# Optimization experiments

Measured on AMD Instinct MI355X. Metric: run time of the kernel, lower is better.

The kernel has to match this reference:

```python
import jax, jax.numpy as jnp
import numpy as np

B, N, C = 8, 1024, 768
H = 12
D = C // H            # 64
HID = int(C * 4.0)    # 3072
SCALE = D ** -0.5
EPS_LN = 1e-5
EPS_BN = 1e-5


def _layernorm(x, g, b):
    mu = jnp.mean(x, axis=-1, keepdims=True)
    var = jnp.mean(jnp.square(x - mu), axis=-1, keepdims=True)
    return (x - mu) * jax.lax.rsqrt(var + EPS_LN) * g + b


def setup_inputs() -> dict:
    key = jax.random.key(0)
    ks = jax.random.split(key, 12)
    s = lambda fan: 1.0 / np.sqrt(fan)
    inp = {
        "inputs": jax.random.normal(ks[0], (B, N, C), jnp.float32),
        "ln1_g": jnp.ones((C,), jnp.float32),
        "ln1_b": jnp.zeros((C,), jnp.float32),
        # nn.Linear(dim, 3*dim, bias=False)
        "qkv_w": jax.random.uniform(ks[1], (3 * C, C), jnp.float32, -s(C), s(C)),
        # nn.Conv2d(H, H, 1, 1) head-mixing matrix
        "conv_w": jax.random.uniform(ks[2], (H, H), jnp.float32, -s(H), s(H)),
        "conv_b": jax.random.uniform(ks[3], (H,), jnp.float32, -s(H), s(H)),
        # BatchNorm2d(H) in eval mode: affine params + running stats
        "bn_g": jnp.ones((H,), jnp.float32),
        "bn_b": jnp.zeros((H,), jnp.float32),
        "bn_rm": jnp.zeros((H,), jnp.float32),
        "bn_rv": jnp.ones((H,), jnp.float32),
        "proj_w": jax.random.uniform(ks[4], (C, C), jnp.float32, -s(C), s(C)),
        "proj_b": jax.random.uniform(ks[5], (C,), jnp.float32, -s(C), s(C)),
        "ln2_g": jnp.ones((C,), jnp.float32),
        "ln2_b": jnp.zeros((C,), jnp.float32),
        "fc1_w": jax.random.uniform(ks[6], (HID, C), jnp.float32, -s(C), s(C)),
        "fc1_b": jax.random.uniform(ks[7], (HID,), jnp.float32, -s(C), s(C)),
        "fc2_w": jax.random.uniform(ks[8], (C, HID), jnp.float32, -s(HID), s(HID)),
        "fc2_b": jax.random.uniform(ks[9], (C,), jnp.float32, -s(HID), s(HID)),
    }
    return inp


def reference(inputs, ln1_g, ln1_b, qkv_w, conv_w, conv_b, bn_g, bn_b, bn_rm, bn_rv,
              proj_w, proj_b, ln2_g, ln2_b, fc1_w, fc1_b, fc2_w, fc2_b):
    # adjust_ratio = 1.0, dropouts are identity (inference), BN uses running stats (eval)
    x_ln = _layernorm(inputs, ln1_g, ln1_b)
    qkv = (x_ln @ qkv_w.T).reshape(B, N, 3, H, D).transpose(2, 0, 3, 1, 4)
    q, k, v = qkv[0], qkv[1], qkv[2]
    attn = jax.nn.softmax(jnp.einsum('bhnd,bhmd->bhnm', q, k) * SCALE, axis=-1)
    # 1x1 conv across heads then BatchNorm2d (eval) * reatten_scale(=1.0)
    attn = jnp.einsum('oh,bhnm->bonm', conv_w, attn) + conv_b[None, :, None, None]
    bn_scale = bn_g * jax.lax.rsqrt(bn_rv + EPS_BN)
    attn = (attn - bn_rm[None, :, None, None]) * bn_scale[None, :, None, None] \
        + bn_b[None, :, None, None]
    attn_next = attn
    out = jnp.einsum('bhnm,bhmd->bhnd', attn, v).transpose(0, 2, 1, 3).reshape(B, N, C)
    out = out @ proj_w.T + proj_b
    x = inputs + out
    h = _layernorm(x, ln2_g, ln2_b)
    h = jax.nn.gelu(h @ fc1_w.T + fc1_b, approximate=False)
    x = x + (h @ fc2_w.T + fc2_b)
    return (x, attn_next)
```

## Files before the change

kernel.cpp:

```cpp
#include <hip/hip_runtime.h>
#include <cmath>

#define B_   8
#define N_   1024
#define C_   768
#define H_   12
#define D_   64
#define HID_ 3072
#define M_   8192

using frag  = __attribute__((ext_vector_type(8))) short;
using f32x4 = __attribute__((ext_vector_type(4))) float;
using s4v   = __attribute__((ext_vector_type(4))) short;

__device__ __forceinline__ short f2bf(float x) {
    union { float f; unsigned u; } v; v.f = x;
    unsigned r = (v.u + 0x7FFFu + ((v.u >> 16) & 1u)) >> 16;
    return (short)r;
}
__device__ __forceinline__ float gelu_exact(float x) {
    return 0.5f * x * (1.0f + erff(x * 0.70710678118654752f));
}
__device__ __forceinline__ void gload16(const void* g, void* l) {
    __builtin_amdgcn_global_load_lds(
        (const __attribute__((address_space(1))) void*)g,
        (__attribute__((address_space(3))) void*)l, 16, 0, 0);
}

__device__ __forceinline__ int2 swz_xy() {
    const int gx = gridDim.x;
    const int nwg = gx * gridDim.y;
    const int orig = blockIdx.y * gx + blockIdx.x;
    const int q = nwg >> 3, r = nwg & 7;
    const int xcd = orig & 7;
    const int base = (xcd < r) ? xcd * (q + 1) : r * (q + 1) + (xcd - r) * q;
    const int wgid = base + (orig >> 3);
    int2 v; v.x = wgid % gx; v.y = wgid / gx;
    return v;
}

#define NW0 (3 * C_ * C_)
#define NW1 (C_ * C_)
#define NW2 (HID_ * C_)
#define NW3 (C_ * HID_)
__global__ __launch_bounds__(256)
void cvt_weights(const float* __restrict__ s0, const float* __restrict__ s1,
                 const float* __restrict__ s2, const float* __restrict__ s3,
                 short* __restrict__ dst)
{
    long i = ((long)blockIdx.x * 256 + threadIdx.x) * 4;
    const float* s; long off;
    if      (i < NW0)             { s = s0; off = i; }
    else if (i < NW0 + NW1)       { s = s1; off = i - NW0; }
    else if (i < NW0 + NW1 + NW2) { s = s2; off = i - NW0 - NW1; }
    else                          { s = s3; off = i - NW0 - NW1 - NW2; }
    float4 u = *(const float4*)(s + off);
    s4v o; o[0] = f2bf(u.x); o[1] = f2bf(u.y); o[2] = f2bf(u.z); o[3] = f2bf(u.w);
    *(s4v*)(dst + i) = o;
}

__global__ __launch_bounds__(256)
void ln_bf16(const float* __restrict__ x, const float* __restrict__ g,
             const float* __restrict__ b, short* __restrict__ y)
{
    __shared__ float red[256];
    const long row = blockIdx.x;
    const float* xr = x + row * C_;
    short* yr = y + row * C_;
    const int t = threadIdx.x;
    float v0 = xr[t], v1 = xr[t + 256], v2 = xr[t + 512];
    red[t] = v0 + v1 + v2;
    __syncthreads();
    for (int o = 128; o > 0; o >>= 1) { if (t < o) red[t] += red[t + o]; __syncthreads(); }
    const float mu = red[0] * (1.0f / 768.0f);
    __syncthreads();
    const float d0 = v0 - mu, d1 = v1 - mu, d2 = v2 - mu;
    red[t] = d0 * d0 + d1 * d1 + d2 * d2;
    __syncthreads();
    for (int o = 128; o > 0; o >>= 1) { if (t < o) red[t] += red[t + o]; __syncthreads(); }
    const float rstd = rsqrtf(red[0] * (1.0f / 768.0f) + 1e-5f);
    yr[t]       = f2bf(d0 * rstd * g[t]       + b[t]);
    yr[t + 256] = f2bf(d1 * rstd * g[t + 256] + b[t + 256]);
    yr[t + 512] = f2bf(d2 * rstd * g[t + 512] + b[t + 512]);
}

template<int BM, int BN, int WGM, int WGN, bool AF32, bool OUTF32,
         bool ACT_GELU, bool STATS, bool CW, bool NTC, int GMODE>
__global__ __launch_bounds__(256)
void gemm_mfma(const void* __restrict__ Ap, int lda, long sAb, long sAh,
               const short* __restrict__ Bp, int ldb, long sBb, long sBh,
               const float* __restrict__ bias,
               const float* __restrict__ res, int ldres,
               void* __restrict__ Cp, int ldc, long sCb, long sCh,
               float2* __restrict__ st,
               int K, float alpha)
{
    constexpr int FM = BM / (WGM * 16), FN = BN / (WGN * 16);
    __shared__ short As[BM * 64];
    __shared__ short Bs[BN * 64];
    const int tid = threadIdx.x;
    const int wid = tid >> 6, lane = tid & 63;
    int bx, by, z;
    if constexpr (GMODE == 1) {
        const int nwg = gridDim.x;
        const int qc = nwg >> 3;
        const int wg = (blockIdx.x & 7) * qc + (blockIdx.x >> 3);
        bx = 0; by = wg & 7; z = wg >> 3;
    } else {
        int2 v = swz_xy(); bx = v.x; by = v.y; z = blockIdx.z;
    }
    const int zb = z / H_, zh = z - zb * H_;
    const long m0 = (long)by * BM;
    const int  n0 = bx * BN;
    const short* Bb = Bp + zb * sBb + zh * sBh + (long)n0 * ldb;
    const short* Abh = nullptr; const float* Afh = nullptr;
    if constexpr (AF32) Afh = (const float*)Ap + zb * sAb + zh * sAh + m0 * lda;
    else                Abh = (const short*)Ap + zb * sAb + zh * sAh + m0 * lda;
    f32x4 acc[FM][FN] = {};
    const int wr = wid / WGN, wc = wid - wr * WGN;
    const int srow = lane >> 3;
    const int schunk = (lane & 7) ^ srow;

    for (int k0 = 0; k0 < K; k0 += 64) {
        if constexpr (!AF32) {
            for (int g = wid; g < BM / 8; g += 4)
                gload16(Abh + (long)(g * 8 + srow) * lda + k0 + schunk * 8, &As[g * 512]);
        } else {
            const int r = tid >> 1, h2 = tid & 1;
            const float* sp = Afh + (long)r * lda + k0 + h2 * 32;
            #pragma unroll
            for (int j = 0; j < 4; ++j) {
                float4 u0 = *(const float4*)(sp + j * 8);
                float4 u1 = *(const float4*)(sp + j * 8 + 4);
                frag w;
                w[0] = f2bf(u0.x); w[1] = f2bf(u0.y); w[2] = f2bf(u0.z); w[3] = f2bf(u0.w);
                w[4] = f2bf(u1.x); w[5] = f2bf(u1.y); w[6] = f2bf(u1.z); w[7] = f2bf(u1.w);
                *(frag*)&As[r * 64 + ((h2 * 4 + j) ^ (r & 7)) * 8] = w;
            }
        }
        for (int g = wid; g < BN / 8; g += 4)
            gload16(Bb + (long)(g * 8 + srow) * ldb + k0 + schunk * 8, &Bs[g * 512]);
        __syncthreads();
        #pragma unroll
        for (int kk = 0; kk < 2; ++kk) {
            frag a[FM], b[FN];
            #pragma unroll
            for (int fm = 0; fm < FM; ++fm) {
                const int r = wr * FM * 16 + fm * 16 + (lane & 15);
                const int ph = (kk * 4 + (lane >> 4)) ^ (r & 7);
                a[fm] = *(const frag*)&As[r * 64 + ph * 8];
            }
            #pragma unroll
            for (int fn = 0; fn < FN; ++fn) {
                const int r = wc * FN * 16 + fn * 16 + (lane & 15);
                const int ph = (kk * 4 + (lane >> 4)) ^ (r & 7);
                b[fn] = *(const frag*)&Bs[r * 64 + ph * 8];
            }
            #pragma unroll
            for (int fm = 0; fm < FM; ++fm)
                #pragma unroll
                for (int fn = 0; fn < FN; ++fn)
                    acc[fm][fn] = __builtin_amdgcn_mfma_f32_16x16x32_bf16(a[fm], b[fn], acc[fm][fn], 0, 0, 0);
        }
        __syncthreads();
    }

    if constexpr (CW) {
        float* Cf = (float*)Cp; short* Cs = (short*)Cp;
        const long cbase = zb * sCb + zh * sCh;
        #pragma unroll
        for (int fm = 0; fm < FM; ++fm) {
            #pragma unroll
            for (int fn = 0; fn < FN; ++fn) {
                const long rg = m0 + wr * FM * 16 + fm * 16 + ((lane >> 4) * 4);
                const int  cg = n0 + wc * FN * 16 + fn * 16 + (lane & 15);
                const float bv = bias ? bias[cg] : 0.0f;
                #pragma unroll
                for (int q = 0; q < 4; ++q) {
                    const long row = rg + q;
                    float v = acc[fm][fn][q] * alpha + bv;
                    if (res) v += res[row * (long)ldres + cg];
                    if constexpr (ACT_GELU) v = gelu_exact(v);
                    if constexpr (OUTF32) {
                        if constexpr (NTC) __builtin_nontemporal_store(v, &Cf[cbase + row * ldc + cg]);
                        else               Cf[cbase + row * ldc + cg] = v;
                    } else {
                        Cs[cbase + row * ldc + cg] = f2bf(v);
                    }
                }
            }
        }
    }

    if constexpr (STATS) {
        float* sred = (float*)As;
        float tmax[FM][4];
        #pragma unroll
        for (int fm = 0; fm < FM; ++fm)
            #pragma unroll
            for (int q = 0; q < 4; ++q) {
                float v = acc[fm][0][q];
                #pragma unroll
                for (int fn = 1; fn < FN; ++fn) v = fmaxf(v, acc[fm][fn][q]);
                v *= alpha;
                v = fmaxf(v, __shfl_xor(v, 1));
                v = fmaxf(v, __shfl_xor(v, 2));
                v = fmaxf(v, __shfl_xor(v, 4));
                v = fmaxf(v, __shfl_xor(v, 8));
                const int r = wr * FM * 16 + fm * 16 + (lane >> 4) * 4 + q;
                if ((lane & 15) == 0) sred[wc * BM + r] = v;
            }
        __syncthreads();
        #pragma unroll
        for (int fm = 0; fm < FM; ++fm)
            #pragma unroll
            for (int q = 0; q < 4; ++q) {
                const int r = wr * FM * 16 + fm * 16 + (lane >> 4) * 4 + q;
                tmax[fm][q] = fmaxf(sred[r], sred[BM + r]);
            }
        __syncthreads();
        #pragma unroll
        for (int fm = 0; fm < FM; ++fm)
            #pragma unroll
            for (int q = 0; q < 4; ++q) {
                float e = 0.0f;
                #pragma unroll
                for (int fn = 0; fn < FN; ++fn)
                    e += __expf(acc[fm][fn][q] * alpha - tmax[fm][q]);
                e += __shfl_xor(e, 1);
                e += __shfl_xor(e, 2);
                e += __shfl_xor(e, 4);
                e += __shfl_xor(e, 8);
                const int r = wr * FM * 16 + fm * 16 + (lane >> 4) * 4 + q;
                if ((lane & 15) == 0) sred[wc * BM + r] = e;
            }
        __syncthreads();
        if (wc == 0) {
            #pragma unroll
            for (int fm = 0; fm < FM; ++fm)
                #pragma unroll
                for (int q = 0; q < 4; ++q) {
                    const int r = wr * FM * 16 + fm * 16 + (lane >> 4) * 4 + q;
                    if ((lane & 15) == 0) {
                        float2 o; o.x = tmax[fm][q]; o.y = sred[r] + sred[BM + r];
                        st[((long)z * N_ + m0 + r) * 8 + bx] = o;
                    }
                }
        }
    }
}

__global__ __launch_bounds__(256)
void qksm(const short* __restrict__ qkvb, const float2* __restrict__ st,
          float* __restrict__ attn,
          const float* __restrict__ cw, const float* __restrict__ cb,
          const float* __restrict__ bg, const float* __restrict__ bb,
          const float* __restrict__ brm, const float* __restrict__ brv)
{
    __shared__ short qs[H_ * 16 * 64];
    __shared__ short ks[2][64 * 64];
    __shared__ float smx[H_][16], sinv[H_][16];
    __shared__ float coef[H_][H_], baseA[H_], scA[H_];
    const int tid = threadIdx.x, wid = tid >> 6, lane = tid & 63;

    const int wg = (blockIdx.x & 7) * 1024 + (blockIdx.x >> 3);
    const int b = wg >> 10, nblk = (wg >> 4) & 63, mblk = wg & 15;
    const int n0 = nblk * 16, m0 = mblk * 64;

    if (tid < H_) {
        const float s = bg[tid] * rsqrtf(brv[tid] + 1e-5f);
        scA[tid] = s;
        baseA[tid] = (cb[tid] - brm[tid]) * s + bb[tid];
    }
    __syncthreads();
    if (tid < H_ * H_) coef[tid / H_][tid % H_] = cw[tid] * scA[tid / H_];
    if (tid < 192) {
        const int h = tid >> 4, r = tid & 15;
        const float2* sp = st + ((long)(b * H_ + h) * N_ + n0 + r) * 8;
        float2 sv[8];
        #pragma unroll
        for (int i = 0; i < 8; ++i) sv[i] = sp[i];
        float gm = sv[0].x;
        #pragma unroll
        for (int i = 1; i < 8; ++i) gm = fmaxf(gm, sv[i].x);
        float gs = 0.0f;
        #pragma unroll
        for (int i = 0; i < 8; ++i) gs += sv[i].y * __expf(sv[i].x - gm);
        smx[h][r] = gm;
        sinv[h][r] = 1.0f / gs;
    }
    __syncthreads();

    const int srow = lane >> 3, schunk = (lane & 7) ^ srow;
    const short* qbase = qkvb + (long)(b * N_ + n0) * (3 * C_);
    for (int g = wid; g < 24; g += 4) {
        const int fr = g * 8 + srow;
        gload16(qbase + (long)(fr & 15) * (3 * C_) + (fr >> 4) * 64 + schunk * 8,
                &qs[g * 512]);
    }
    const short* kbase = qkvb + C_ + (long)(b * N_ + m0) * (3 * C_);
    for (int g = wid; g < 8; g += 4) {
        const int fr = g * 8 + srow;
        gload16(kbase + (long)fr * (3 * C_) + schunk * 8, &ks[0][g * 512]);
    }

    float macc[H_][4] = {};
    const int rowb = (lane >> 4) * 4;
    const int colw = wid * 16 + (lane & 15);

    for (int h = 0; h < H_; ++h) {
        asm volatile("s_waitcnt vmcnt(0)" ::: "memory");
        __builtin_amdgcn_sched_barrier(0);
        __builtin_amdgcn_s_barrier();
        if (h < H_ - 1) {
            for (int g = wid; g < 8; g += 4) {
                const int fr = g * 8 + srow;
                gload16(kbase + (long)fr * (3 * C_) + (h + 1) * 64 + schunk * 8,
                        &ks[(h + 1) & 1][g * 512]);
            }
        }
        f32x4 acc = {};
        const int afr = h * 16 + (lane & 15);
        const int bfr = colw;
        #pragma unroll
        for (int kk = 0; kk < 2; ++kk) {
            const frag a  = *(const frag*)&qs[afr * 64 + (((kk * 4 + (lane >> 4)) ^ (afr & 7))) * 8];
            const frag bv = *(const frag*)&ks[h & 1][bfr * 64 + (((kk * 4 + (lane >> 4)) ^ (bfr & 7))) * 8];
            acc = __builtin_amdgcn_mfma_f32_16x16x32_bf16(a, bv, acc, 0, 0, 0);
        }
        #pragma unroll
        for (int q = 0; q < 4; ++q) {
            const float e = __expf(acc[q] * 0.125f - smx[h][rowb + q]) * sinv[h][rowb + q];
            #pragma unroll
            for (int o = 0; o < H_; ++o) macc[o][q] += coef[o][h] * e;
        }
    }

    #pragma unroll
    for (int o = 0; o < H_; ++o) {
        float* ap = attn + ((long)(b * H_ + o) << 20) + ((long)(n0 + rowb) << 10) + m0 + colw;
        #pragma unroll
        for (int q = 0; q < 4; ++q)
            __builtin_nontemporal_store(macc[o][q] + baseA[o], ap + ((long)q << 10));
    }
}

__global__ __launch_bounds__(256)
void vtrans(const short* __restrict__ qkv, short* __restrict__ vT)
{
    __shared__ short tile[64][72];
    const int bh = blockIdx.x;
    const int n0 = blockIdx.y * 64;
    const int b = bh / H_, h = bh - b * H_;
    const short* src = qkv + (long)b * N_ * (3 * C_) + 2 * C_ + h * D_;
    const int t = threadIdx.x;
    {
        const int r = t >> 2, c = (t & 3) * 16;
        const short* sp = src + (long)(n0 + r) * (3 * C_) + c;
        #pragma unroll
        for (int j = 0; j < 16; j++) tile[r][c + j] = sp[j];
    }
    __syncthreads();
    {
        const int d = t >> 2, c = (t & 3) * 16;
        short* dp = vT + (long)bh * (D_ * N_) + (long)d * N_ + n0 + c;
        #pragma unroll
        for (int j = 0; j < 16; j++) dp[j] = tile[c + j][d];
    }
}

extern "C" void kernel_launch(void* const* d_in, const int* in_sizes, int n_in,
                              void* d_out, int out_size, void* d_ws, size_t ws_size,
                              hipStream_t stream)
{
    const float* inp    = (const float*)d_in[0];
    const float* ln1_g  = (const float*)d_in[1];
    const float* ln1_b  = (const float*)d_in[2];
    const float* qkv_w  = (const float*)d_in[3];
    const float* conv_w = (const float*)d_in[4];
    const float* conv_b = (const float*)d_in[5];
    const float* bn_g   = (const float*)d_in[6];
    const float* bn_b   = (const float*)d_in[7];
    const float* bn_rm  = (const float*)d_in[8];
    const float* bn_rv  = (const float*)d_in[9];
    const float* proj_w = (const float*)d_in[10];
    const float* proj_b = (const float*)d_in[11];
    const float* ln2_g  = (const float*)d_in[12];
    const float* ln2_b  = (const float*)d_in[13];
    const float* fc1_w  = (const float*)d_in[14];
    const float* fc1_b  = (const float*)d_in[15];
    const float* fc2_w  = (const float*)d_in[16];
    const float* fc2_b  = (const float*)d_in[17];

    float* outx = (float*)d_out;
    float* attn = outx + (long)M_ * C_;

    char* w = (char*)d_ws;
    short* wqkv  = (short*)w;  w += (long)NW0 * 2;
    short* wproj = (short*)w;  w += (long)NW1 * 2;
    short* wfc1  = (short*)w;  w += (long)NW2 * 2;
    short* wfc2  = (short*)w;  w += (long)NW3 * 2;
    short* xln   = (short*)w;  w += (long)M_ * C_ * 2;
    short* qkvb  = (short*)w;
    short* hbuf  = qkvb;       w += (long)M_ * HID_ * 2;
    short* vT    = (short*)w;  w += (long)B_ * H_ * D_ * N_ * 2;
    short* Obf   = (short*)w;  w += (long)M_ * C_ * 2;
    float* xres  = (float*)w;  w += (long)M_ * C_ * 4;
    float2* st   = (float2*)w; w += (long)B_ * H_ * N_ * 8 * 8;

    cvt_weights<<<(NW0 + NW1 + NW2 + NW3) / 1024, 256, 0, stream>>>(
        qkv_w, proj_w, fc1_w, fc2_w, wqkv);

    ln_bf16<<<M_, 256, 0, stream>>>(inp, ln1_g, ln1_b, xln);

    gemm_mfma<128, 128, 2, 2, false, false, false, false, true, false, 0>
        <<<dim3(18, 64, 1), 256, 0, stream>>>(
        xln, C_, 0, 0, wqkv, C_, 0, 0, nullptr, nullptr, 0,
        qkvb, 3 * C_, 0, 0, nullptr, C_, 1.0f);

    vtrans<<<dim3(B_ * H_, 16), 256, 0, stream>>>(qkvb, vT);

    gemm_mfma<128, 128, 2, 2, false, false, false, true, false, false, 0>
        <<<dim3(8, 8, 96), 256, 0, stream>>>(
        qkvb,      3 * C_, (long)N_ * 3 * C_, D_,
        qkvb + C_, 3 * C_, (long)N_ * 3 * C_, D_,
        nullptr, nullptr, 0,
        nullptr, N_, 0, 0, st, D_, 0.125f);

    qksm<<<8192, 256, 0, stream>>>(qkvb, st, attn,
                                   conv_w, conv_b, bn_g, bn_b, bn_rm, bn_rv);

    gemm_mfma<128, 64, 4, 1, true, false, false, false, true, false, 1>
        <<<dim3(768, 1, 1), 256, 0, stream>>>(
        attn, N_, (long)H_ * N_ * N_, (long)N_ * N_,
        vT, N_, (long)H_ * D_ * N_, (long)D_ * N_,
        nullptr, nullptr, 0,
        Obf, C_, (long)N_ * C_, D_, nullptr, N_, 1.0f);

    gemm_mfma<128, 64, 4, 1, false, true, false, false, true, false, 0>
        <<<dim3(12, 64, 1), 256, 0, stream>>>(
        Obf, C_, 0, 0, wproj, C_, 0, 0, proj_b, inp, C_,
        xres, C_, 0, 0, nullptr, C_, 1.0f);

    ln_bf16<<<M_, 256, 0, stream>>>(xres, ln2_g, ln2_b, xln);

    gemm_mfma<128, 128, 2, 2, false, false, true, false, true, false, 0>
        <<<dim3(24, 64, 1), 256, 0, stream>>>(
        xln, C_, 0, 0, wfc1, C_, 0, 0, fc1_b, nullptr, 0,
        hbuf, HID_, 0, 0, nullptr, C_, 1.0f);

    gemm_mfma<128, 64, 4, 1, false, true, false, false, true, true, 0>
        <<<dim3(12, 64, 1), 256, 0, stream>>>(
        hbuf, HID_, 0, 0, wfc2, HID_, 0, 0, fc2_b, xres, C_,
        outx, C_, 0, 0, nullptr, HID_, 1.0f);
}
```

Measured before the change: 545.0 us.

## Emit bf16 copy of attention in qksm and feed PV GEMM from it

```diff
diff --git a/kernel.cpp b/kernel.cpp
--- a/kernel.cpp
+++ b/kernel.cpp
@@ -84,10 +84,10 @@
     yr[t + 512] = f2bf(d2 * rstd * g[t + 512] + b[t + 512]);
 }
 
-template<int BM, int BN, int WGM, int WGN, bool AF32, bool OUTF32,
+template<int BM, int BN, int WGM, int WGN, bool OUTF32,
          bool ACT_GELU, bool STATS, bool CW, bool NTC, int GMODE>
 __global__ __launch_bounds__(256)
-void gemm_mfma(const void* __restrict__ Ap, int lda, long sAb, long sAh,
+void gemm_mfma(const short* __restrict__ Ap, int lda, long sAb, long sAh,
                const short* __restrict__ Bp, int ldb, long sBb, long sBh,
                const float* __restrict__ bias,
                const float* __restrict__ res, int ldres,
@@ -112,32 +112,16 @@
     const int zb = z / H_, zh = z - zb * H_;
     const long m0 = (long)by * BM;
     const int  n0 = bx * BN;
+    const short* Ab = Ap + zb * sAb + zh * sAh + m0 * lda;
     const short* Bb = Bp + zb * sBb + zh * sBh + (long)n0 * ldb;
-    const short* Abh = nullptr; const float* Afh = nullptr;
-    if constexpr (AF32) Afh = (const float*)Ap + zb * sAb + zh * sAh + m0 * lda;
-    else                Abh = (const short*)Ap + zb * sAb + zh * sAh + m0 * lda;
     f32x4 acc[FM][FN] = {};
     const int wr = wid / WGN, wc = wid - wr * WGN;
     const int srow = lane >> 3;
     const int schunk = (lane & 7) ^ srow;
 
     for (int k0 = 0; k0 < K; k0 += 64) {
-        if constexpr (!AF32) {
-            for (int g = wid; g < BM / 8; g += 4)
-                gload16(Abh + (long)(g * 8 + srow) * lda + k0 + schunk * 8, &As[g * 512]);
-        } else {
-            const int r = tid >> 1, h2 = tid & 1;
-            const float* sp = Afh + (long)r * lda + k0 + h2 * 32;
-            #pragma unroll
-            for (int j = 0; j < 4; ++j) {
-                float4 u0 = *(const float4*)(sp + j * 8);
-                float4 u1 = *(const float4*)(sp + j * 8 + 4);
-                frag w;
-                w[0] = f2bf(u0.x); w[1] = f2bf(u0.y); w[2] = f2bf(u0.z); w[3] = f2bf(u0.w);
-                w[4] = f2bf(u1.x); w[5] = f2bf(u1.y); w[6] = f2bf(u1.z); w[7] = f2bf(u1.w);
-                *(frag*)&As[r * 64 + ((h2 * 4 + j) ^ (r & 7)) * 8] = w;
-            }
-        }
+        for (int g = wid; g < BM / 8; g += 4)
+            gload16(Ab + (long)(g * 8 + srow) * lda + k0 + schunk * 8, &As[g * 512]);
         for (int g = wid; g < BN / 8; g += 4)
             gload16(Bb + (long)(g * 8 + srow) * ldb + k0 + schunk * 8, &Bs[g * 512]);
         __syncthreads();
@@ -252,7 +236,7 @@
 
 __global__ __launch_bounds__(256)
 void qksm(const short* __restrict__ qkvb, const float2* __restrict__ st,
-          float* __restrict__ attn,
+          float* __restrict__ attn, short* __restrict__ Pbuf,
           const float* __restrict__ cw, const float* __restrict__ cb,
           const float* __restrict__ bg, const float* __restrict__ bb,
           const float* __restrict__ brm, const float* __restrict__ brv)
@@ -336,12 +320,32 @@
         }
     }
 
+    __syncthreads();
+    float* obuf = (float*)qs;
+    short* pbuf = (short*)ks;
+    const int rr = tid >> 4, cc = (tid & 15) * 4;
     #pragma unroll
-    for (int o = 0; o < H_; ++o) {
-        float* ap = attn + ((long)(b * H_ + o) << 20) + ((long)(n0 + rowb) << 10) + m0 + colw;
-        #pragma unroll
-        for (int q = 0; q < 4; ++q)
-            __builtin_nontemporal_store(macc[o][q] + baseA[o], ap + ((long)q << 10));
+    for (int ob = 0; ob < 2; ++ob) {
+        #pragma unroll
+        for (int hh = 0; hh < 6; ++hh) {
+            const int o = ob * 6 + hh;
+            #pragma unroll
+            for (int q = 0; q < 4; ++q) {
+                const float v = macc[o][q] + baseA[o];
+                obuf[hh * 1024 + (rowb + q) * 64 + colw] = v;
+                pbuf[hh * 1024 + (rowb + q) * 64 + colw] = f2bf(v);
+            }
+        }
+        __syncthreads();
+        #pragma unroll
+        for (int hh = 0; hh < 6; ++hh) {
+            const int o = ob * 6 + hh;
+            const long pl = ((long)(b * H_ + o) << 20) + ((long)(n0 + rr) << 10) + m0 + cc;
+            const f32x4 ov = *(const f32x4*)&obuf[hh * 1024 + rr * 64 + cc];
+            __builtin_nontemporal_store(ov, (f32x4*)(attn + pl));
+            *(s4v*)(Pbuf + pl) = *(const s4v*)&pbuf[hh * 1024 + rr * 64 + cc];
+        }
+        __syncthreads();
     }
 }
 
@@ -407,49 +411,50 @@
     short* Obf   = (short*)w;  w += (long)M_ * C_ * 2;
     float* xres  = (float*)w;  w += (long)M_ * C_ * 4;
     float2* st   = (float2*)w; w += (long)B_ * H_ * N_ * 8 * 8;
+    short* Pbuf  = (short*)w;  w += (long)B_ * H_ * N_ * N_ * 2;
 
     cvt_weights<<<(NW0 + NW1 + NW2 + NW3) / 1024, 256, 0, stream>>>(
         qkv_w, proj_w, fc1_w, fc2_w, wqkv);
 
     ln_bf16<<<M_, 256, 0, stream>>>(inp, ln1_g, ln1_b, xln);
 
-    gemm_mfma<128, 128, 2, 2, false, false, false, false, true, false, 0>
+    gemm_mfma<128, 128, 2, 2, false, false, false, true, false, 0>
         <<<dim3(18, 64, 1), 256, 0, stream>>>(
         xln, C_, 0, 0, wqkv, C_, 0, 0, nullptr, nullptr, 0,
         qkvb, 3 * C_, 0, 0, nullptr, C_, 1.0f);
 
     vtrans<<<dim3(B_ * H_, 16), 256, 0, stream>>>(qkvb, vT);
 
-    gemm_mfma<128, 128, 2, 2, false, false, false, true, false, false, 0>
+    gemm_mfma<128, 128, 2, 2, false, false, true, false, false, 0>
         <<<dim3(8, 8, 96), 256, 0, stream>>>(
         qkvb,      3 * C_, (long)N_ * 3 * C_, D_,
         qkvb + C_, 3 * C_, (long)N_ * 3 * C_, D_,
         nullptr, nullptr, 0,
         nullptr, N_, 0, 0, st, D_, 0.125f);
 
-    qksm<<<8192, 256, 0, stream>>>(qkvb, st, attn,
+    qksm<<<8192, 256, 0, stream>>>(qkvb, st, attn, Pbuf,
                                    conv_w, conv_b, bn_g, bn_b, bn_rm, bn_rv);
 
-    gemm_mfma<128, 64, 4, 1, true, false, false, false, true, false, 1>
+    gemm_mfma<128, 64, 4, 1, false, false, false, true, false, 1>
         <<<dim3(768, 1, 1), 256, 0, stream>>>(
-        attn, N_, (long)H_ * N_ * N_, (long)N_ * N_,
+        Pbuf, N_, (long)H_ * N_ * N_, (long)N_ * N_,
         vT, N_, (long)H_ * D_ * N_, (long)D_ * N_,
         nullptr, nullptr, 0,
         Obf, C_, (long)N_ * C_, D_, nullptr, N_, 1.0f);
 
-    gemm_mfma<128, 64, 4, 1, false, true, false, false, true, false, 0>
+    gemm_mfma<128, 64, 4, 1, true, false, false, true, false, 0>
         <<<dim3(12, 64, 1), 256, 0, stream>>>(
         Obf, C_, 0, 0, wproj, C_, 0, 0, proj_b, inp, C_,
         xres, C_, 0, 0, nullptr, C_, 1.0f);
 
     ln_bf16<<<M_, 256, 0, stream>>>(xres, ln2_g, ln2_b, xln);
 
-    gemm_mfma<128, 128, 2, 2, false, false, true, false, true, false, 0>
+    gemm_mfma<128, 128, 2, 2, false, true, false, true, false, 0>
         <<<dim3(24, 64, 1), 256, 0, stream>>>(
         xln, C_, 0, 0, wfc1, C_, 0, 0, fc1_b, nullptr, 0,
         hbuf, HID_, 0, 0, nullptr, C_, 1.0f);
 
-    gemm_mfma<128, 64, 4, 1, false, true, false, false, true, true, 0>
+    gemm_mfma<128, 64, 4, 1, true, false, false, true, true, 0>
         <<<dim3(12, 64, 1), 256, 0, stream>>>(
         hbuf, HID_, 0, 0, wfc2, HID_, 0, 0, fc2_b, xres, C_,
         outx, C_, 0, 0, nullptr, HID_, 1.0f);
```

Result: no change. 543.1 us (median of 2 runs) (-0.4%).

## Fuse attention-value product into head-mixing softmax kernel with split-K partials

Applied to the files above, without the earlier changes.

```diff
diff --git a/kernel.cpp b/kernel.cpp
--- a/kernel.cpp
+++ b/kernel.cpp
@@ -84,10 +84,11 @@
     yr[t + 512] = f2bf(d2 * rstd * g[t + 512] + b[t + 512]);
 }
 
-template<int BM, int BN, int WGM, int WGN, bool AF32, bool OUTF32,
+template<int BM, int BN, int WGM, int WGN, bool AF32S, bool OUTF32,
          bool ACT_GELU, bool STATS, bool CW, bool NTC, int GMODE>
 __global__ __launch_bounds__(256)
-void gemm_mfma(const void* __restrict__ Ap, int lda, long sAb, long sAh,
+void gemm_mfma(const void* __restrict__ Ap, const float* __restrict__ Ap2,
+               int lda, long sAb, long sAh,
                const short* __restrict__ Bp, int ldb, long sBb, long sBh,
                const float* __restrict__ bias,
                const float* __restrict__ res, int ldres,
@@ -113,28 +114,31 @@
     const long m0 = (long)by * BM;
     const int  n0 = bx * BN;
     const short* Bb = Bp + zb * sBb + zh * sBh + (long)n0 * ldb;
-    const short* Abh = nullptr; const float* Afh = nullptr;
-    if constexpr (AF32) Afh = (const float*)Ap + zb * sAb + zh * sAh + m0 * lda;
-    else                Abh = (const short*)Ap + zb * sAb + zh * sAh + m0 * lda;
+    const short* Abh = nullptr; const float* Af0 = nullptr; const float* Af1 = nullptr;
+    if constexpr (AF32S) { Af0 = (const float*)Ap + m0 * lda; Af1 = Ap2 + m0 * lda; }
+    else                 Abh = (const short*)Ap + zb * sAb + zh * sAh + m0 * lda;
     f32x4 acc[FM][FN] = {};
     const int wr = wid / WGN, wc = wid - wr * WGN;
     const int srow = lane >> 3;
     const int schunk = (lane & 7) ^ srow;
 
     for (int k0 = 0; k0 < K; k0 += 64) {
-        if constexpr (!AF32) {
+        if constexpr (!AF32S) {
             for (int g = wid; g < BM / 8; g += 4)
                 gload16(Abh + (long)(g * 8 + srow) * lda + k0 + schunk * 8, &As[g * 512]);
         } else {
             const int r = tid >> 1, h2 = tid & 1;
-            const float* sp = Afh + (long)r * lda + k0 + h2 * 32;
+            const float* sp0 = Af0 + (long)r * lda + k0 + h2 * 32;
+            const float* sp1 = Af1 + (long)r * lda + k0 + h2 * 32;
             #pragma unroll
             for (int j = 0; j < 4; ++j) {
-                float4 u0 = *(const float4*)(sp + j * 8);
-                float4 u1 = *(const float4*)(sp + j * 8 + 4);
+                f32x4 a0 = *(const f32x4*)(sp0 + j * 8);
+                f32x4 a1 = *(const f32x4*)(sp0 + j * 8 + 4);
+                f32x4 b0 = *(const f32x4*)(sp1 + j * 8);
+                f32x4 b1 = *(const f32x4*)(sp1 + j * 8 + 4);
                 frag w;
-                w[0] = f2bf(u0.x); w[1] = f2bf(u0.y); w[2] = f2bf(u0.z); w[3] = f2bf(u0.w);
-                w[4] = f2bf(u1.x); w[5] = f2bf(u1.y); w[6] = f2bf(u1.z); w[7] = f2bf(u1.w);
+                #pragma unroll
+                for (int e = 0; e < 4; ++e) { w[e] = f2bf(a0[e] + b0[e]); w[e + 4] = f2bf(a1[e] + b1[e]); }
                 *(frag*)&As[r * 64 + ((h2 * 4 + j) ^ (r & 7)) * 8] = w;
             }
         }
@@ -251,21 +255,24 @@
 }
 
 __global__ __launch_bounds__(256)
-void qksm(const short* __restrict__ qkvb, const float2* __restrict__ st,
-          float* __restrict__ attn,
-          const float* __restrict__ cw, const float* __restrict__ cb,
-          const float* __restrict__ bg, const float* __restrict__ bb,
-          const float* __restrict__ brm, const float* __restrict__ brv)
+void qksmpv(const short* __restrict__ qkvb, const short* __restrict__ vT,
+            const float2* __restrict__ st,
+            float* __restrict__ attn, float* __restrict__ Opart,
+            const float* __restrict__ cw, const float* __restrict__ cb,
+            const float* __restrict__ bg, const float* __restrict__ bb,
+            const float* __restrict__ brm, const float* __restrict__ brv)
 {
     __shared__ short qs[H_ * 16 * 64];
-    __shared__ short ks[2][64 * 64];
+    __shared__ short ring[2][64 * 64];
+    __shared__ short pm[4 * 16 * 64];
     __shared__ float smx[H_][16], sinv[H_][16];
     __shared__ float coef[H_][H_], baseA[H_], scA[H_];
     const int tid = threadIdx.x, wid = tid >> 6, lane = tid & 63;
 
-    const int wg = (blockIdx.x & 7) * 1024 + (blockIdx.x >> 3);
-    const int b = wg >> 10, nblk = (wg >> 4) & 63, mblk = wg & 15;
-    const int n0 = nblk * 16, m0 = mblk * 64;
+    const int wg = (blockIdx.x & 7) * 128 + (blockIdx.x >> 3);
+    const int b = wg >> 7, rem = wg & 127;
+    const int nblk = rem >> 1, mhalf = rem & 1;
+    const int n0 = nblk * 16, mbase = mhalf * 512;
 
     if (tid < H_) {
         const float s = bg[tid] * rsqrtf(brv[tid] + 1e-5f);
@@ -298,50 +305,115 @@
         gload16(qbase + (long)(fr & 15) * (3 * C_) + (fr >> 4) * 64 + schunk * 8,
                 &qs[g * 512]);
     }
-    const short* kbase = qkvb + C_ + (long)(b * N_ + m0) * (3 * C_);
-    for (int g = wid; g < 8; g += 4) {
-        const int fr = g * 8 + srow;
-        gload16(kbase + (long)fr * (3 * C_) + schunk * 8, &ks[0][g * 512]);
-    }
-
-    float macc[H_][4] = {};
+    const short* kcol = qkvb + C_;
+    {
+        const short* kb = kcol + (long)(b * N_ + mbase) * (3 * C_);
+        for (int g = wid; g < 8; g += 4)
+            gload16(kb + (long)(g * 8 + srow) * (3 * C_) + schunk * 8, &ring[0][g * 512]);
+    }
+
+    f32x4 oacc[H_] = {};
     const int rowb = (lane >> 4) * 4;
     const int colw = wid * 16 + (lane & 15);
-
-    for (int h = 0; h < H_; ++h) {
-        asm volatile("s_waitcnt vmcnt(0)" ::: "memory");
-        __builtin_amdgcn_sched_barrier(0);
-        __builtin_amdgcn_s_barrier();
-        if (h < H_ - 1) {
-            for (int g = wid; g < 8; g += 4) {
-                const int fr = g * 8 + srow;
-                gload16(kbase + (long)fr * (3 * C_) + (h + 1) * 64 + schunk * 8,
-                        &ks[(h + 1) & 1][g * 512]);
-            }
-        }
-        f32x4 acc = {};
-        const int afr = h * 16 + (lane & 15);
-        const int bfr = colw;
-        #pragma unroll
-        for (int kk = 0; kk < 2; ++kk) {
-            const frag a  = *(const frag*)&qs[afr * 64 + (((kk * 4 + (lane >> 4)) ^ (afr & 7))) * 8];
-            const frag bv = *(const frag*)&ks[h & 1][bfr * 64 + (((kk * 4 + (lane >> 4)) ^ (bfr & 7))) * 8];
-            acc = __builtin_amdgcn_mfma_f32_16x16x32_bf16(a, bv, acc, 0, 0, 0);
-        }
-        #pragma unroll
-        for (int q = 0; q < 4; ++q) {
-            const float e = __expf(acc[q] * 0.125f - smx[h][rowb + q]) * sinv[h][rowb + q];
-            #pragma unroll
-            for (int o = 0; o < H_; ++o) macc[o][q] += coef[o][h] * e;
-        }
-    }
-
+    const long vbb = (long)b * H_ * (D_ * N_);
+    int t = 0;
+
+    for (int mc = 0; mc < 8; ++mc) {
+        const int mo = mbase + mc * 64;
+        const short* kb = kcol + (long)(b * N_ + mo) * (3 * C_);
+        float macc[H_][4] = {};
+
+        #pragma unroll 1
+        for (int h = 0; h < H_; ++h) {
+            asm volatile("s_waitcnt vmcnt(0)" ::: "memory");
+            __builtin_amdgcn_sched_barrier(0);
+            __builtin_amdgcn_s_barrier();
+            if (h < H_ - 1) {
+                for (int g = wid; g < 8; g += 4)
+                    gload16(kb + (long)(g * 8 + srow) * (3 * C_) + (h + 1) * 64 + schunk * 8,
+                            &ring[(t + 1) & 1][g * 512]);
+            } else {
+                const short* vb = vT + vbb + mo;
+                for (int g = wid; g < 8; g += 4)
+                    gload16(vb + (long)(g * 8 + srow) * N_ + schunk * 8,
+                            &ring[(t + 1) & 1][g * 512]);
+            }
+            f32x4 acc = {};
+            const int afr = h * 16 + (lane & 15);
+            #pragma unroll
+            for (int kk = 0; kk < 2; ++kk) {
+                const frag a  = *(const frag*)&qs[afr * 64 + (((kk * 4 + (lane >> 4)) ^ (afr & 7))) * 8];
+                const frag bv = *(const frag*)&ring[t & 1][colw * 64 + (((kk * 4 + (lane >> 4)) ^ (colw & 7))) * 8];
+                acc = __builtin_amdgcn_mfma_f32_16x16x32_bf16(a, bv, acc, 0, 0, 0);
+            }
+            #pragma unroll
+            for (int q = 0; q < 4; ++q) {
+                const float e = __expf(acc[q] * 0.125f - smx[h][rowb + q]) * sinv[h][rowb + q];
+                #pragma unroll
+                for (int o = 0; o < H_; ++o) macc[o][q] += coef[o][h] * e;
+            }
+            ++t;
+        }
+
+        #pragma unroll
+        for (int o = 0; o < H_; ++o) {
+            float* ap = attn + ((long)(b * H_ + o) << 20) + ((long)(n0 + rowb) << 10) + mo + colw;
+            #pragma unroll
+            for (int q = 0; q < 4; ++q)
+                __builtin_nontemporal_store(macc[o][q] + baseA[o], ap + ((long)q << 10));
+        }
+
+        #pragma unroll
+        for (int pass = 0; pass < 3; ++pass) {
+            asm volatile("s_waitcnt lgkmcnt(0)" ::: "memory");
+            __builtin_amdgcn_sched_barrier(0);
+            __builtin_amdgcn_s_barrier();
+            #pragma unroll
+            for (int ol = 0; ol < 4; ++ol) {
+                const int o = pass * 4 + ol;
+                #pragma unroll
+                for (int q = 0; q < 4; ++q) {
+                    const int row = ol * 16 + rowb + q;
+                    const int ch = (colw >> 3) ^ (row & 7);
+                    pm[row * 64 + ch * 8 + (colw & 7)] = f2bf(macc[o][q] + baseA[o]);
+                }
+            }
+            #pragma unroll
+            for (int ov = 0; ov < 4; ++ov) {
+                const int o = pass * 4 + ov;
+                asm volatile("s_waitcnt vmcnt(0) lgkmcnt(0)" ::: "memory");
+                __builtin_amdgcn_sched_barrier(0);
+                __builtin_amdgcn_s_barrier();
+                if (o < H_ - 1) {
+                    const short* vb = vT + vbb + (long)(o + 1) * (D_ * N_) + mo;
+                    for (int g = wid; g < 8; g += 4)
+                        gload16(vb + (long)(g * 8 + srow) * N_ + schunk * 8,
+                                &ring[(t + 1) & 1][g * 512]);
+                } else if (mc < 7) {
+                    const short* kb2 = kcol + (long)(b * N_ + mbase + (mc + 1) * 64) * (3 * C_);
+                    for (int g = wid; g < 8; g += 4)
+                        gload16(kb2 + (long)(g * 8 + srow) * (3 * C_) + schunk * 8,
+                                &ring[(t + 1) & 1][g * 512]);
+                }
+                #pragma unroll
+                for (int kk = 0; kk < 2; ++kk) {
+                    const int ar = ov * 16 + (lane & 15);
+                    const frag a  = *(const frag*)&pm[ar * 64 + (((kk * 4 + (lane >> 4)) ^ (ar & 7))) * 8];
+                    const int br = wid * 16 + (lane & 15);
+                    const frag bv = *(const frag*)&ring[t & 1][br * 64 + (((kk * 4 + (lane >> 4)) ^ (br & 7))) * 8];
+                    oacc[o] = __builtin_amdgcn_mfma_f32_16x16x32_bf16(a, bv, oacc[o], 0, 0, 0);
+                }
+                ++t;
+            }
+        }
+    }
+
+    float* op = Opart + (long)mhalf * M_ * C_;
     #pragma unroll
     for (int o = 0; o < H_; ++o) {
-        float* ap = attn + ((long)(b * H_ + o) << 20) + ((long)(n0 + rowb) << 10) + m0 + colw;
         #pragma unroll
         for (int q = 0; q < 4; ++q)
-            __builtin_nontemporal_store(macc[o][q] + baseA[o], ap + ((long)q << 10));
+            op[(long)(b * N_ + n0 + rowb + q) * C_ + o * D_ + wid * 16 + (lane & 15)] = oacc[o][q];
     }
 }
 
@@ -404,9 +476,9 @@
     short* qkvb  = (short*)w;
     short* hbuf  = qkvb;       w += (long)M_ * HID_ * 2;
     short* vT    = (short*)w;  w += (long)B_ * H_ * D_ * N_ * 2;
-    short* Obf   = (short*)w;  w += (long)M_ * C_ * 2;
     float* xres  = (float*)w;  w += (long)M_ * C_ * 4;
     float2* st   = (float2*)w; w += (long)B_ * H_ * N_ * 8 * 8;
+    float* Opart = (float*)w;  w += (long)2 * M_ * C_ * 4;
 
     cvt_weights<<<(NW0 + NW1 + NW2 + NW3) / 1024, 256, 0, stream>>>(
         qkv_w, proj_w, fc1_w, fc2_w, wqkv);
@@ -415,42 +487,36 @@
 
     gemm_mfma<128, 128, 2, 2, false, false, false, false, true, false, 0>
         <<<dim3(18, 64, 1), 256, 0, stream>>>(
-        xln, C_, 0, 0, wqkv, C_, 0, 0, nullptr, nullptr, 0,
+        xln, nullptr, C_, 0, 0, wqkv, C_, 0, 0, nullptr, nullptr, 0,
         qkvb, 3 * C_, 0, 0, nullptr, C_, 1.0f);
 
     vtrans<<<dim3(B_ * H_, 16), 256, 0, stream>>>(qkvb, vT);
 
     gemm_mfma<128, 128, 2, 2, false, false, false, true, false, false, 0>
         <<<dim3(8, 8, 96), 256, 0, stream>>>(
-        qkvb,      3 * C_, (long)N_ * 3 * C_, D_,
-        qkvb + C_, 3 * C_, (long)N_ * 3 * C_, D_,
+        qkvb, nullptr, 3 * C_, (long)N_ * 3 * C_, D_,
+        qkvb + C_,     3 * C_, (long)N_ * 3 * C_, D_,
         nullptr, nullptr, 0,
         nullptr, N_, 0, 0, st, D_, 0.125f);
 
-    qksm<<<8192, 256, 0, stream>>>(qkvb, st, attn,
-                                   conv_w, conv_b, bn_g, bn_b, bn_rm, bn_rv);
-
-    gemm_mfma<128, 64, 4, 1, true, false, false, false, true, false, 1>
-        <<<dim3(768, 1, 1), 256, 0, stream>>>(
-        attn, N_, (long)H_ * N_ * N_, (long)N_ * N_,
-        vT, N_, (long)H_ * D_ * N_, (long)D_ * N_,
-        nullptr, nullptr, 0,
-        Obf, C_, (long)N_ * C_, D_, nullptr, N_, 1.0f);
-
-    gemm_mfma<128, 64, 4, 1, false, true, false, false, true, false, 0>
+    qksmpv<<<1024, 256, 0, stream>>>(qkvb, vT, st, attn, Opart,
+                                     conv_w, conv_b, bn_g, bn_b, bn_rm, bn_rv);
+
+    gemm_mfma<128, 64, 4, 1, true, true, false, false, true, false, 0>
         <<<dim3(12, 64, 1), 256, 0, stream>>>(
-        Obf, C_, 0, 0, wproj, C_, 0, 0, proj_b, inp, C_,
+        Opart, Opart + (long)M_ * C_, C_, 0, 0,
+        wproj, C_, 0, 0, proj_b, inp, C_,
         xres, C_, 0, 0, nullptr, C_, 1.0f);
 
     ln_bf16<<<M_, 256, 0, stream>>>(xres, ln2_g, ln2_b, xln);
 
     gemm_mfma<128, 128, 2, 2, false, false, true, false, true, false, 0>
         <<<dim3(24, 64, 1), 256, 0, stream>>>(
-        xln, C_, 0, 0, wfc1, C_, 0, 0, fc1_b, nullptr, 0,
+        xln, nullptr, C_, 0, 0, wfc1, C_, 0, 0, fc1_b, nullptr, 0,
         hbuf, HID_, 0, 0, nullptr, C_, 1.0f);
 
     gemm_mfma<128, 64, 4, 1, false, true, false, false, true, true, 0>
         <<<dim3(12, 64, 1), 256, 0, stream>>>(
-        hbuf, HID_, 0, 0, wfc2, HID_, 0, 0, fc2_b, xres, C_,
+        hbuf, nullptr, HID_, 0, 0, wfc2, HID_, 0, 0, fc2_b, xres, C_,
         outx, C_, 0, 0, nullptr, HID_, 1.0f);
 }
```

Measured after the change: 623.6 us. +14.4%, slower.
